# Kernel tuning notes

Measured on AMD Instinct MI355X. Metric: run time of the kernel, lower is better.

The kernel has to match this reference:

```python
import jax, jax.numpy as jnp
import numpy as np

_ALIAS = {11: 11, 13: 11, 16: 11, 21: 21, 22: 21, 23: 21, 31: 31, 32: 31, 33: 31,
          41: 41, 42: 41, 43: 41, 44: 41, 51: 51, 52: 51, 53: 51}
_COMPAT = {11: (11, 13, 16), 21: (14, 15, 21, 22, 23), 31: (15, 31, 32, 33),
           41: (41, 42, 43, 44), 51: (15, 51, 52, 53)}
_VOCAB = 64


def _tables():
    alias = np.full((_VOCAB,), -1, np.int32)
    for k, v in _ALIAS.items():
        alias[k] = v
    compat = np.zeros((_VOCAB, _VOCAB), np.float32)
    has = np.zeros((_VOCAB,), np.bool_)
    for r, toks in _COMPAT.items():
        has[r] = True
        for t in toks:
            compat[r, t] = 1.0
    return jnp.asarray(alias), jnp.asarray(compat), jnp.asarray(has)


def setup_inputs() -> dict:
    key = jax.random.key(0)
    k1, k2, k3, k4 = jax.random.split(key, 4)
    B, T, D, A, S, TTL = 8, 4096, 1024, 32, 16, 64
    H = max(TTL * 4, S * 4)
    hidden = jax.random.normal(k1, (B, T, D), jnp.float32)
    anchor_repr = jax.random.normal(k2, (B, A, D), jnp.float32)
    input_ids = jax.random.randint(k3, (B, T), 0, _VOCAB, jnp.int32)
    # end_idx in [S-1, T-H) so span start >= 0 and full horizon fits in T
    anchor_end = jax.random.randint(k4, (B, A), S - 1, T - H, jnp.int32)
    return {"hidden": hidden, "anchor_repr": anchor_repr, "input_ids": input_ids,
            "anchor_end": anchor_end, "span_len": S, "ttl": TTL}


def reference(hidden, anchor_repr, input_ids, anchor_end, span_len, ttl):
    alias_t, compat_t, has_t = _tables()
    B, T, D = hidden.shape
    A = anchor_end.shape[1]
    S = int(span_len)
    H = max(int(ttl) * 4, S * 4)
    W = H - S + 1
    eps = 1e-8

    bidx = jnp.arange(B)[:, None, None]
    start = anchor_end + 1                                   # [B,A]
    fut_idx = start[..., None] + jnp.arange(H)               # [B,A,H]
    future = hidden[bidx, fut_idx]                           # [B,A,H,D]
    fut_tok = input_ids[bidx, fut_idx]                       # [B,A,H]
    span_idx = (anchor_end - S + 1)[..., None] + jnp.arange(S)
    span = input_ids[bidx, span_idx]                         # [B,A,S]
    anchor_tok = input_ids[jnp.arange(B)[:, None], anchor_end]  # [B,A]

    # hidden-space stats (cosine_similarity with F.cosine_similarity eps)
    mean_future = future.mean(axis=2)                        # [B,A,D]
    nr = jnp.maximum(jnp.linalg.norm(anchor_repr, axis=-1), eps)
    nf = jnp.maximum(jnp.linalg.norm(mean_future, axis=-1), eps)
    sim = (anchor_repr * mean_future).sum(-1) / (nr * nf)    # [B,A]
    future_shift = jnp.linalg.norm(future - anchor_repr[:, :, None, :], axis=-1).mean(-1)
    hidden_c = jnp.maximum(0.0, (1.0 - sim) / 2.0)
    token_c = 1.0 - (fut_tok == anchor_tok[..., None]).astype(jnp.float32).mean(-1)

    # sliding windows over the horizon
    win_idx = jnp.arange(W)[:, None] + jnp.arange(S)[None, :]  # [W,S]
    win = fut_tok[:, :, win_idx]                               # [B,A,W,S]
    eq = (win == span[:, :, None, :]).astype(jnp.float32)     # [B,A,W,S]
    exact = eq.mean(-1)                                       # [B,A,W]
    pos_w = jnp.linspace(1.0, 0.4, S)
    pos_w = pos_w / pos_w.sum()
    positional = (eq * pos_w).sum(-1)

    # set-overlap: count distinct anchor tokens present in window
    eqmat = span[..., :, None] == span[..., None, :]          # [B,A,S,S]
    tri = jnp.tril(jnp.ones((S, S), bool), -1)
    first_occ = ~(eqmat & tri).any(-1)                        # first occurrence mask
    first_f = first_occ.astype(jnp.float32)
    denom = first_f.sum(-1)                                   # |set(anchor_span)|
    in_win = (win[..., :, None] == span[:, :, None, None, :]).any(-2)  # [B,A,W,S]
    overlap = (in_win.astype(jnp.float32) * first_f[:, :, None, :]).sum(-1) / denom[:, :, None]

    # infer_reference_root: first aliased token, else mode (smallest on ties)
    alias_span = alias_t[span]                                # [B,A,S], -1 if no alias
    has_a = alias_span >= 0
    first_i = jnp.argmax(has_a, -1)
    first_root = jnp.take_along_axis(alias_span, first_i[..., None], -1)[..., 0]
    counts = eqmat.sum(-1)
    maxc = counts.max(-1, keepdims=True)
    mode = jnp.where(counts == maxc, span, _VOCAB).min(-1)
    root = jnp.where(has_a.any(-1), first_root, mode)         # [B,A]

    r4 = root[:, :, None, None]
    root_pers = (win == r4).astype(jnp.float32).mean(-1)      # [B,A,W]
    alias_c = (alias_t[win] == r4).astype(jnp.float32).mean(-1)
    hard = compat_t[r4, win].mean(-1)
    regime = jnp.where(has_t[root][:, :, None],
                       0.55 * hard + 0.2 * overlap + 0.15 * alias_c + 0.1 * root_pers,
                       0.45 * exact + 0.3 * overlap + 0.1 * alias_c + 0.15 * root_pers)

    sims = 0.25 * exact + 0.15 * overlap + 0.35 * positional + 0.25 * regime
    best = sims.max(-1)
    mrp = root_pers.mean(-1)
    mrc = regime.mean(-1)
    dmass = (sims >= 0.6).astype(jnp.float32).mean(-1)
    dcoh = 0.6 * sims.mean(-1) + 0.25 * mrp + 0.15 * mrc
    pattern_c = 1.0 - (0.6 * best + 0.2 * mrp + 0.2 * mrc)

    contr = jnp.clip(0.2 * hidden_c + 0.2 * token_c + 0.6 * pattern_c, 0.0, 1.0)
    # [8,B,A]: contradiction, future_shift, similarity, hidden_c, token_c, pattern_c, mass, coherence
    return jnp.stack([contr, future_shift, sim, hidden_c, token_c, pattern_c, dmass, dcoh], 0)
```

## Files before the change

### kernel.cpp

```cpp
#include <hip/hip_runtime.h>
#include <math.h>

constexpr int kB = 8;
constexpr int kT = 4096;
constexpr int kD = 1024;
constexpr int kA = 32;
constexpr int kS = 16;
constexpr int kH = 256;
constexpr int kW = kH - kS + 1;
constexpr int NC = kD / 256;

constexpr int SPLIT = 8;
constexpr int RPS   = kH / SPLIT;
constexpr int NT1   = 256;
constexpr int NW1   = NT1 / 64;
constexpr int NWG1  = kB * kA * SPLIT;
constexpr int NT2   = 256;
constexpr int NW2   = NT2 / 64;

constexpr int NTF = 512;
constexpr int NWF = NTF / 64;

__device__ inline float wredsum(float v) {
#pragma unroll
    for (int m = 32; m >= 1; m >>= 1) v += __shfl_xor(v, m, 64);
    return v;
}
__device__ inline float wredmax(float v) {
#pragma unroll
    for (int m = 32; m >= 1; m >>= 1) v = fmaxf(v, __shfl_xor(v, m, 64));
    return v;
}

__device__ inline int alias_of(int t) {
    switch (t) {
        case 11: case 13: case 16: return 11;
        case 21: case 22: case 23: return 21;
        case 31: case 32: case 33: return 31;
        case 41: case 42: case 43: case 44: return 41;
        case 51: case 52: case 53: return 51;
        default: return -1;
    }
}

__global__ __launch_bounds__(NT1, 4) void phaseA_kernel(
    const float* __restrict__ hidden,
    const float* __restrict__ anchor_repr,
    const int*   __restrict__ anchor_end,
    float*       __restrict__ partial,
    float*       __restrict__ pshift)
{
    __shared__ float smean[NW1][kD];
    __shared__ float swshift[NW1];

    const int id = blockIdx.x;
    const int lb = (id & 7) * (NWG1 / 8) + (id >> 3);
    const int ba    = lb / SPLIT;
    const int slice = lb % SPLIT;
    const int b     = ba / kA;
    const int tid  = threadIdx.x;
    const int lane = tid & 63;
    const int wave = tid >> 6;

    const int e     = anchor_end[ba];
    const int start = e + 1;

    const float* arow = anchor_repr + (size_t)ba * kD;
    float4 anc[NC];
#pragma unroll
    for (int c = 0; c < NC; ++c) anc[c] = *(const float4*)(arow + 256 * c + 4 * lane);

    const float* hbase =
        hidden + ((size_t)b * kT + start + slice * RPS) * kD + 4 * lane;

    float sum[NC][4];
#pragma unroll
    for (int c = 0; c < NC; ++c)
#pragma unroll
        for (int j = 0; j < 4; ++j) sum[c][j] = 0.f;

    float shift_acc = 0.f;
    for (int hh = 0; hh < RPS; hh += 2 * NW1) {
        const float* r0 = hbase + (size_t)(hh + wave) * kD;
        const float* r1 = hbase + (size_t)(hh + wave + NW1) * kD;
        float ss0 = 0.f, ss1 = 0.f;
#pragma unroll
        for (int c = 0; c < NC; ++c) {
            float4 x0 = *(const float4*)(r0 + 256 * c);
            float4 x1 = *(const float4*)(r1 + 256 * c);
            float4 a  = anc[c];
            sum[c][0] += x0.x + x1.x;
            sum[c][1] += x0.y + x1.y;
            sum[c][2] += x0.z + x1.z;
            sum[c][3] += x0.w + x1.w;
            float d0 = x0.x - a.x, d1 = x0.y - a.y, d2 = x0.z - a.z, d3 = x0.w - a.w;
            float g0 = x1.x - a.x, g1 = x1.y - a.y, g2 = x1.z - a.z, g3 = x1.w - a.w;
            ss0 += d0*d0 + d1*d1 + d2*d2 + d3*d3;
            ss1 += g0*g0 + g1*g1 + g2*g2 + g3*g3;
        }
        ss0 = wredsum(ss0);
        ss1 = wredsum(ss1);
        shift_acc += sqrtf(ss0) + sqrtf(ss1);
    }
#pragma unroll
    for (int c = 0; c < NC; ++c)
        *(float4*)&smean[wave][256 * c + 4 * lane] =
            make_float4(sum[c][0], sum[c][1], sum[c][2], sum[c][3]);
    if (lane == 0) swshift[wave] = shift_acc;
    __syncthreads();

    float4 t = make_float4(0.f, 0.f, 0.f, 0.f);
#pragma unroll
    for (int w = 0; w < NW1; ++w) {
        const float4 p = *(const float4*)&smean[w][4 * tid];
        t.x += p.x; t.y += p.y; t.z += p.z; t.w += p.w;
    }
    *(float4*)(partial + ((size_t)lb << 10) + 4 * tid) = t;
    if (tid == 0) {
        float s = 0.f;
#pragma unroll
        for (int w = 0; w < NW1; ++w) s += swshift[w];
        pshift[lb] = s;
    }
}

__global__ __launch_bounds__(NT2, 1) void phaseB_kernel(
    const float* __restrict__ anchor_repr,
    const int*   __restrict__ input_ids,
    const int*   __restrict__ anchor_end,
    const float* __restrict__ partial,
    const float* __restrict__ pshift,
    float*       __restrict__ out)
{
    __shared__ int   sfut[kH];
    __shared__ int   sspan[kS];
    __shared__ float sposw[kS];
    __shared__ float sr1[NW2], sr2[NW2], sr3[NW2], sr4[NW2], sr5[NW2];
    __shared__ float s_sim, s_shift, s_hidc, s_tokc;
    __shared__ int   s_root, s_has;
    __shared__ unsigned long long s_spanmask, s_amask, s_hmask;
    __shared__ float s_denom;

    const int ba   = blockIdx.x;
    const int b    = ba / kA;
    const int tid  = threadIdx.x;
    const int lane = tid & 63;
    const int wave = tid >> 6;

    const int e     = anchor_end[ba];
    const int start = e + 1;
    const int* ids  = input_ids + b * kT;
    const int anchor_tok = ids[e];

    sfut[tid] = ids[start + tid];
    if (tid < kS) {
        sspan[tid] = ids[e - kS + 1 + tid];
        sposw[tid] = (1.0f - 0.04f * (float)tid) * (1.0f / 11.2f);
    }

    const float* arow = anchor_repr + (size_t)ba * kD;
    float4 acc = make_float4(0.f, 0.f, 0.f, 0.f);
#pragma unroll
    for (int s = 0; s < SPLIT; ++s) {
        const float4 p =
            *(const float4*)(partial + (((size_t)ba * SPLIT + s) << 10) + 4 * tid);
        acc.x += p.x; acc.y += p.y; acc.z += p.z; acc.w += p.w;
    }
    const float4 av = *(const float4*)(arow + 4 * tid);
    const float inv_h = 1.0f / (float)kH;
    float mx = acc.x * inv_h, my = acc.y * inv_h, mz = acc.z * inv_h, mw = acc.w * inv_h;
    float pm2  = mx*mx + my*my + mz*mz + mw*mw;
    float pdot = mx*av.x + my*av.y + mz*av.z + mw*av.w;
    float pa2  = av.x*av.x + av.y*av.y + av.z*av.z + av.w*av.w;
    float peq  = (sfut[tid] == anchor_tok) ? 1.f : 0.f;
    pm2 = wredsum(pm2); pdot = wredsum(pdot); pa2 = wredsum(pa2); peq = wredsum(peq);
    if (lane == 0) { sr1[wave] = pm2; sr2[wave] = pdot; sr3[wave] = pa2; sr4[wave] = peq; }
    __syncthreads();

    if (tid == 0) {
        float m2 = 0.f, dt = 0.f, a2 = 0.f, eqc = 0.f;
        for (int w = 0; w < NW2; ++w) { m2 += sr1[w]; dt += sr2[w]; a2 += sr3[w]; eqc += sr4[w]; }
        float shift = 0.f;
        for (int s = 0; s < SPLIT; ++s) shift += pshift[ba * SPLIT + s];
        float nf = fmaxf(sqrtf(m2), 1e-8f);
        float nr = fmaxf(sqrtf(a2), 1e-8f);
        float sim = dt / (nr * nf);
        s_sim   = sim;
        s_shift = shift * (1.0f / kH);
        s_hidc  = fmaxf(0.f, (1.f - sim) * 0.5f);
        s_tokc  = 1.f - eqc * (1.0f / kH);
    }
    if (tid == 64) {
        unsigned long long spanmask = 0;
        for (int s = 0; s < kS; ++s) spanmask |= 1ull << sspan[s];
        int root = -1;
        for (int s = 0; s < kS; ++s) { int al = alias_of(sspan[s]); if (al >= 0) { root = al; break; } }
        if (root < 0) {
            int counts[kS], maxc = 0;
            for (int s = 0; s < kS; ++s) {
                int c = 0;
                for (int s2 = 0; s2 < kS; ++s2) c += (sspan[s2] == sspan[s]) ? 1 : 0;
                counts[s] = c; if (c > maxc) maxc = c;
            }
            int mode = 64;
            for (int s = 0; s < kS; ++s) if (counts[s] == maxc && sspan[s] < mode) mode = sspan[s];
            root = mode;
        }
        unsigned long long am = 0, hm = 0; int has = 0;
        switch (root) {
            case 11: am = (1ull<<11)|(1ull<<13)|(1ull<<16);            hm = am;                       has = 1; break;
            case 21: am = (1ull<<21)|(1ull<<22)|(1ull<<23);            hm = am|(1ull<<14)|(1ull<<15); has = 1; break;
            case 31: am = (1ull<<31)|(1ull<<32)|(1ull<<33);            hm = am|(1ull<<15);            has = 1; break;
            case 41: am = (1ull<<41)|(1ull<<42)|(1ull<<43)|(1ull<<44); hm = am;                       has = 1; break;
            case 51: am = (1ull<<51)|(1ull<<52)|(1ull<<53);            hm = am|(1ull<<15);            has = 1; break;
            default: break;
        }
        s_root = root; s_has = has; s_spanmask = spanmask; s_amask = am; s_hmask = hm;
        s_denom = (float)__popcll(spanmask);
    }
    __syncthreads();

    const int root = s_root, has = s_has;
    const unsigned long long spanmask = s_spanmask, amask = s_amask, hmask = s_hmask;
    const float inv_denom = 1.0f / s_denom;

    float sims = -1e30f, rootpers = 0.f, regime = 0.f, simsum = 0.f, cnt = 0.f;
    if (tid < kW) {
        float wex = 0.f, wpos = 0.f, wrp = 0.f, wal = 0.f, whard = 0.f;
        unsigned long long wm = 0;
#pragma unroll
        for (int s = 0; s < kS; ++s) {
            int tok = sfut[tid + s];
            wm |= 1ull << tok;
            bool eq = (tok == sspan[s]);
            wex  += eq ? 1.f : 0.f;
            wpos += eq ? sposw[s] : 0.f;
            wrp  += (tok == root) ? 1.f : 0.f;
            wal  += ((amask >> tok) & 1ull) ? 1.f : 0.f;
            whard += ((hmask >> tok) & 1ull) ? 1.f : 0.f;
        }
        float exact  = wex * (1.f / kS);
        float overlap = (float)__popcll(wm & spanmask) * inv_denom;
        rootpers = wrp * (1.f / kS);
        float aliasc = wal * (1.f / kS);
        float hard   = whard * (1.f / kS);
        regime = has ? (0.55f*hard  + 0.2f*overlap + 0.15f*aliasc + 0.1f*rootpers)
                     : (0.45f*exact + 0.3f*overlap + 0.1f*aliasc  + 0.15f*rootpers);
        sims = 0.25f*exact + 0.15f*overlap + 0.35f*wpos + 0.25f*regime;
        simsum = sims;
        cnt = (sims >= 0.6f) ? 1.f : 0.f;
    }
    float rmax = wredmax(sims);
    float rsum = wredsum(simsum);
    float rrp  = wredsum(rootpers);
    float rreg = wredsum(regime);
    float rcnt = wredsum(cnt);
    if (lane == 0) { sr1[wave] = rmax; sr2[wave] = rsum; sr3[wave] = rrp; sr4[wave] = rreg; sr5[wave] = rcnt; }
    __syncthreads();

    if (tid == 0) {
        float best = -1e30f, ssum = 0.f, srp = 0.f, sreg = 0.f, scnt = 0.f;
        for (int w = 0; w < NW2; ++w) {
            best = fmaxf(best, sr1[w]); ssum += sr2[w]; srp += sr3[w]; sreg += sr4[w]; scnt += sr5[w];
        }
        const float invW = 1.0f / (float)kW;
        float msims = ssum * invW, mrp = srp * invW, mrc = sreg * invW, dmass = scnt * invW;
        float dcoh      = 0.6f*msims + 0.25f*mrp + 0.15f*mrc;
        float pattern_c = 1.f - (0.6f*best + 0.2f*mrp + 0.2f*mrc);
        float contr     = 0.2f*s_hidc + 0.2f*s_tokc + 0.6f*pattern_c;
        contr = fminf(fmaxf(contr, 0.f), 1.f);
        const int n = kB * kA;
        out[0*n + ba] = contr;
        out[1*n + ba] = s_shift;
        out[2*n + ba] = s_sim;
        out[3*n + ba] = s_hidc;
        out[4*n + ba] = s_tokc;
        out[5*n + ba] = pattern_c;
        out[6*n + ba] = dmass;
        out[7*n + ba] = dcoh;
    }
}

__global__ __launch_bounds__(NTF, 1) void monitor_kernel(
    const float* __restrict__ hidden,
    const float* __restrict__ anchor_repr,
    const int*   __restrict__ input_ids,
    const int*   __restrict__ anchor_end,
    float*       __restrict__ out)
{
    __shared__ float smean[NWF][kD];
    __shared__ int   sfut[kH];
    __shared__ int   sspan[kS];
    __shared__ float sposw[kS];
    __shared__ float sr1[NWF], sr2[NWF], sr3[NWF], sr4[NWF], sr5[NWF];
    __shared__ float s_sim, s_shift, s_hidc, s_tokc;
    __shared__ int   s_root, s_has;
    __shared__ unsigned long long s_spanmask, s_amask, s_hmask;
    __shared__ float s_denom;

    const int ba   = blockIdx.x;
    const int b    = ba / kA;
    const int tid  = threadIdx.x;
    const int lane = tid & 63;
    const int wave = tid >> 6;

    const int e     = anchor_end[ba];
    const int start = e + 1;
    const int* ids  = input_ids + b * kT;
    const int anchor_tok = ids[e];

    if (tid < kH) sfut[tid] = ids[start + tid];
    if (tid < kS) {
        sspan[tid] = ids[e - kS + 1 + tid];
        sposw[tid] = (1.0f - 0.04f * (float)tid) * (1.0f / 11.2f);
    }

    const float* arow = anchor_repr + (size_t)ba * kD;
    float4 anc[NC];
#pragma unroll
    for (int c = 0; c < NC; ++c) anc[c] = *(const float4*)(arow + 256 * c + 4 * lane);
    const float* hbase = hidden + ((size_t)b * kT + start) * kD + 4 * lane;

    float sum[NC][4];
#pragma unroll
    for (int c = 0; c < NC; ++c)
#pragma unroll
        for (int j = 0; j < 4; ++j) sum[c][j] = 0.f;

    float shift_acc = 0.f;
    for (int h = wave; h < kH; h += 2 * NWF) {
        const float* r0 = hbase + (size_t)h * kD;
        const float* r1 = hbase + (size_t)(h + NWF) * kD;
        float ss0 = 0.f, ss1 = 0.f;
#pragma unroll
        for (int c = 0; c < NC; ++c) {
            float4 x0 = *(const float4*)(r0 + 256 * c);
            float4 x1 = *(const float4*)(r1 + 256 * c);
            float4 a  = anc[c];
            sum[c][0] += x0.x + x1.x;
            sum[c][1] += x0.y + x1.y;
            sum[c][2] += x0.z + x1.z;
            sum[c][3] += x0.w + x1.w;
            float d0 = x0.x - a.x, d1 = x0.y - a.y, d2 = x0.z - a.z, d3 = x0.w - a.w;
            float g0 = x1.x - a.x, g1 = x1.y - a.y, g2 = x1.z - a.z, g3 = x1.w - a.w;
            ss0 += d0*d0 + d1*d1 + d2*d2 + d3*d3;
            ss1 += g0*g0 + g1*g1 + g2*g2 + g3*g3;
        }
        ss0 = wredsum(ss0);
        ss1 = wredsum(ss1);
        shift_acc += sqrtf(ss0) + sqrtf(ss1);
    }
#pragma unroll
    for (int c = 0; c < NC; ++c)
#pragma unroll
        for (int j = 0; j < 4; ++j) smean[wave][256 * c + 4 * lane + j] = sum[c][j];
    if (lane == 0) sr1[wave] = shift_acc;
    __syncthreads();

    float pm2 = 0.f, pdot = 0.f, pa2 = 0.f;
#pragma unroll
    for (int j = 0; j < kD / NTF; ++j) {
        int d = tid * (kD / NTF) + j;
        float tot = 0.f;
#pragma unroll
        for (int w2 = 0; w2 < NWF; ++w2) tot += smean[w2][d];
        float m  = tot * (1.0f / kH);
        float av = arow[d];
        pm2 += m * m; pdot += m * av; pa2 += av * av;
    }
    float peq = (tid < kH && sfut[tid] == anchor_tok) ? 1.f : 0.f;
    pm2 = wredsum(pm2); pdot = wredsum(pdot); pa2 = wredsum(pa2); peq = wredsum(peq);
    if (lane == 0) { sr2[wave] = pm2; sr3[wave] = pdot; sr4[wave] = pa2; sr5[wave] = peq; }
    __syncthreads();

    if (tid == 0) {
        float shift = 0.f, m2 = 0.f, dt = 0.f, a2 = 0.f, eqc = 0.f;
        for (int w2 = 0; w2 < NWF; ++w2) {
            shift += sr1[w2]; m2 += sr2[w2]; dt += sr3[w2]; a2 += sr4[w2]; eqc += sr5[w2];
        }
        float nf = fmaxf(sqrtf(m2), 1e-8f);
        float nr = fmaxf(sqrtf(a2), 1e-8f);
        float sim = dt / (nr * nf);
        s_sim   = sim;
        s_shift = shift * (1.0f / kH);
        s_hidc  = fmaxf(0.f, (1.f - sim) * 0.5f);
        s_tokc  = 1.f - eqc * (1.0f / kH);
    }
    if (tid == 64) {
        unsigned long long spanmask = 0;
        for (int s = 0; s < kS; ++s) spanmask |= 1ull << sspan[s];
        int root = -1;
        for (int s = 0; s < kS; ++s) { int al = alias_of(sspan[s]); if (al >= 0) { root = al; break; } }
        if (root < 0) {
            int counts[kS], maxc = 0;
            for (int s = 0; s < kS; ++s) {
                int c = 0;
                for (int s2 = 0; s2 < kS; ++s2) c += (sspan[s2] == sspan[s]) ? 1 : 0;
                counts[s] = c; if (c > maxc) maxc = c;
            }
            int mode = 64;
            for (int s = 0; s < kS; ++s) if (counts[s] == maxc && sspan[s] < mode) mode = sspan[s];
            root = mode;
        }
        unsigned long long am = 0, hm = 0; int has = 0;
        switch (root) {
            case 11: am = (1ull<<11)|(1ull<<13)|(1ull<<16);            hm = am;                       has = 1; break;
            case 21: am = (1ull<<21)|(1ull<<22)|(1ull<<23);            hm = am|(1ull<<14)|(1ull<<15); has = 1; break;
            case 31: am = (1ull<<31)|(1ull<<32)|(1ull<<33);            hm = am|(1ull<<15);            has = 1; break;
            case 41: am = (1ull<<41)|(1ull<<42)|(1ull<<43)|(1ull<<44); hm = am;                       has = 1; break;
            case 51: am = (1ull<<51)|(1ull<<52)|(1ull<<53);            hm = am|(1ull<<15);            has = 1; break;
            default: break;
        }
        s_root = root; s_has = has; s_spanmask = spanmask; s_amask = am; s_hmask = hm;
        s_denom = (float)__popcll(spanmask);
    }
    __syncthreads();

    const int root = s_root, has = s_has;
    const unsigned long long spanmask = s_spanmask, amask = s_amask, hmask = s_hmask;
    const float inv_denom = 1.0f / s_denom;

    float sims = -1e30f, rootpers = 0.f, regime = 0.f, simsum = 0.f, cnt = 0.f;
    if (tid < kW) {
        float wex = 0.f, wpos = 0.f, wrp = 0.f, wal = 0.f, whard = 0.f;
        unsigned long long wm = 0;
#pragma unroll
        for (int s = 0; s < kS; ++s) {
            int tok = sfut[tid + s];
            wm |= 1ull << tok;
            bool eq = (tok == sspan[s]);
            wex  += eq ? 1.f : 0.f;
            wpos += eq ? sposw[s] : 0.f;
            wrp  += (tok == root) ? 1.f : 0.f;
            wal  += ((amask >> tok) & 1ull) ? 1.f : 0.f;
            whard += ((hmask >> tok) & 1ull) ? 1.f : 0.f;
        }
        float exact  = wex * (1.f / kS);
        float overlap = (float)__popcll(wm & spanmask) * inv_denom;
        rootpers = wrp * (1.f / kS);
        float aliasc = wal * (1.f / kS);
        float hard   = whard * (1.f / kS);
        regime = has ? (0.55f*hard  + 0.2f*overlap + 0.15f*aliasc + 0.1f*rootpers)
                     : (0.45f*exact + 0.3f*overlap + 0.1f*aliasc  + 0.15f*rootpers);
        sims = 0.25f*exact + 0.15f*overlap + 0.35f*wpos + 0.25f*regime;
        simsum = sims;
        cnt = (sims >= 0.6f) ? 1.f : 0.f;
    }
    float rmax = wredmax(sims);
    float rsum = wredsum(simsum);
    float rrp  = wredsum(rootpers);
    float rreg = wredsum(regime);
    float rcnt = wredsum(cnt);
    if (lane == 0) { sr1[wave] = rmax; sr2[wave] = rsum; sr3[wave] = rrp; sr4[wave] = rreg; sr5[wave] = rcnt; }
    __syncthreads();

    if (tid == 0) {
        float best = -1e30f, ssum = 0.f, srp = 0.f, sreg = 0.f, scnt = 0.f;
        for (int w2 = 0; w2 < NWF; ++w2) {
            best = fmaxf(best, sr1[w2]); ssum += sr2[w2]; srp += sr3[w2]; sreg += sr4[w2]; scnt += sr5[w2];
        }
        const float invW = 1.0f / (float)kW;
        float msims = ssum * invW, mrp = srp * invW, mrc = sreg * invW, dmass = scnt * invW;
        float dcoh      = 0.6f*msims + 0.25f*mrp + 0.15f*mrc;
        float pattern_c = 1.f - (0.6f*best + 0.2f*mrp + 0.2f*mrc);
        float contr     = 0.2f*s_hidc + 0.2f*s_tokc + 0.6f*pattern_c;
        contr = fminf(fmaxf(contr, 0.f), 1.f);
        const int n = kB * kA;
        out[0*n + ba] = contr;
        out[1*n + ba] = s_shift;
        out[2*n + ba] = s_sim;
        out[3*n + ba] = s_hidc;
        out[4*n + ba] = s_tokc;
        out[5*n + ba] = pattern_c;
        out[6*n + ba] = dmass;
        out[7*n + ba] = dcoh;
    }
}

extern "C" void kernel_launch(void* const* d_in, const int* in_sizes, int n_in,
                              void* d_out, int out_size, void* d_ws, size_t ws_size,
                              hipStream_t stream) {
    const float* hidden      = (const float*)d_in[0];
    const float* anchor_repr = (const float*)d_in[1];
    const int*   input_ids   = (const int*)d_in[2];
    const int*   anchor_end  = (const int*)d_in[3];
    float* out = (float*)d_out;

    const size_t n_partial = (size_t)NWG1 * kD;
    const size_t need      = (n_partial + NWG1) * sizeof(float);

    if (d_ws != nullptr && ws_size >= need) {
        float* partial = (float*)d_ws;
        float* pshift  = partial + n_partial;
        hipLaunchKernelGGL(phaseA_kernel, dim3(NWG1), dim3(NT1), 0, stream,
                           hidden, anchor_repr, anchor_end, partial, pshift);
        hipLaunchKernelGGL(phaseB_kernel, dim3(kB * kA), dim3(NT2), 0, stream,
                           anchor_repr, input_ids, anchor_end, partial, pshift, out);
    } else {
        hipLaunchKernelGGL(monitor_kernel, dim3(kB * kA), dim3(NTF), 0, stream,
                           hidden, anchor_repr, input_ids, anchor_end, out);
    }
}
```

Baseline: 215.1 us.

## Tile hidden rows per batch and share loads across overlapping anchor windows

The first stage is restructured so that each block owns a fixed 128-row tile of one batch's hidden states, not one slice of one anchor's window. The block loads each row once and accumulates it into every anchor window that covers it, up to eight anchors per pass, keeping the anchor vectors in shared memory. The aim is to remove the redundant global reads caused by overlapping 256-row windows. The cost is more branching, several block-wide syncs per anchor pair, and serial passes when many anchors hit one tile. The second stage and the fallback kernel move to 1024-thread blocks and sum up to three partials per anchor.

```diff
diff --git a/kernel.cpp b/kernel.cpp
--- a/kernel.cpp
+++ b/kernel.cpp
@@ -8,18 +8,14 @@
 constexpr int kS = 16;
 constexpr int kH = 256;
 constexpr int kW = kH - kS + 1;
+constexpr int kBA = kB * kA;
+constexpr int kRB = 128;
+constexpr int kNJ = kT / kRB;
+constexpr int kMK = 3;
 constexpr int NC = kD / 256;
 
-constexpr int SPLIT = 8;
-constexpr int RPS   = kH / SPLIT;
-constexpr int NT1   = 256;
-constexpr int NW1   = NT1 / 64;
-constexpr int NWG1  = kB * kA * SPLIT;
-constexpr int NT2   = 256;
-constexpr int NW2   = NT2 / 64;
-
-constexpr int NTF = 512;
-constexpr int NWF = NTF / 64;
+constexpr int NT = 1024;
+constexpr int NW = NT / 64;
 
 __device__ inline float wredsum(float v) {
 #pragma unroll
@@ -43,88 +39,136 @@
     }
 }
 
-__global__ __launch_bounds__(NT1, 4) void phaseA_kernel(
+__global__ __launch_bounds__(NT) void s1_kernel(
     const float* __restrict__ hidden,
     const float* __restrict__ anchor_repr,
     const int*   __restrict__ anchor_end,
     float*       __restrict__ partial,
     float*       __restrict__ pshift)
 {
-    __shared__ float smean[NW1][kD];
-    __shared__ float swshift[NW1];
+    __shared__ float lanc[8][kD];
+    __shared__ float comb[NW][kD];
+    __shared__ float ssh[NW];
 
     const int id = blockIdx.x;
-    const int lb = (id & 7) * (NWG1 / 8) + (id >> 3);
-    const int ba    = lb / SPLIT;
-    const int slice = lb % SPLIT;
-    const int b     = ba / kA;
+    const int b  = id & 7;
+    const int j  = id >> 3;
     const int tid  = threadIdx.x;
     const int lane = tid & 63;
     const int wave = tid >> 6;
-
-    const int e     = anchor_end[ba];
-    const int start = e + 1;
-
-    const float* arow = anchor_repr + (size_t)ba * kD;
-    float4 anc[NC];
-#pragma unroll
-    for (int c = 0; c < NC; ++c) anc[c] = *(const float4*)(arow + 256 * c + 4 * lane);
-
-    const float* hbase =
-        hidden + ((size_t)b * kT + start + slice * RPS) * kD + 4 * lane;
-
-    float sum[NC][4];
-#pragma unroll
-    for (int c = 0; c < NC; ++c)
-#pragma unroll
-        for (int j = 0; j < 4; ++j) sum[c][j] = 0.f;
-
-    float shift_acc = 0.f;
-    for (int hh = 0; hh < RPS; hh += 2 * NW1) {
-        const float* r0 = hbase + (size_t)(hh + wave) * kD;
-        const float* r1 = hbase + (size_t)(hh + wave + NW1) * kD;
-        float ss0 = 0.f, ss1 = 0.f;
-#pragma unroll
-        for (int c = 0; c < NC; ++c) {
-            float4 x0 = *(const float4*)(r0 + 256 * c);
-            float4 x1 = *(const float4*)(r1 + 256 * c);
-            float4 a  = anc[c];
-            sum[c][0] += x0.x + x1.x;
-            sum[c][1] += x0.y + x1.y;
-            sum[c][2] += x0.z + x1.z;
-            sum[c][3] += x0.w + x1.w;
-            float d0 = x0.x - a.x, d1 = x0.y - a.y, d2 = x0.z - a.z, d3 = x0.w - a.w;
-            float g0 = x1.x - a.x, g1 = x1.y - a.y, g2 = x1.z - a.z, g3 = x1.w - a.w;
-            ss0 += d0*d0 + d1*d1 + d2*d2 + d3*d3;
-            ss1 += g0*g0 + g1*g1 + g2*g2 + g3*g3;
-        }
-        ss0 = wredsum(ss0);
-        ss1 = wredsum(ss1);
-        shift_acc += sqrtf(ss0) + sqrtf(ss1);
-    }
-#pragma unroll
-    for (int c = 0; c < NC; ++c)
-        *(float4*)&smean[wave][256 * c + 4 * lane] =
-            make_float4(sum[c][0], sum[c][1], sum[c][2], sum[c][3]);
-    if (lane == 0) swshift[wave] = shift_acc;
-    __syncthreads();
-
-    float4 t = make_float4(0.f, 0.f, 0.f, 0.f);
-#pragma unroll
-    for (int w = 0; w < NW1; ++w) {
-        const float4 p = *(const float4*)&smean[w][4 * tid];
-        t.x += p.x; t.y += p.y; t.z += p.z; t.w += p.w;
-    }
-    *(float4*)(partial + ((size_t)lb << 10) + 4 * tid) = t;
-    if (tid == 0) {
-        float s = 0.f;
-#pragma unroll
-        for (int w = 0; w < NW1; ++w) s += swshift[w];
-        pshift[lb] = s;
-    }
-}
-
-__global__ __launch_bounds__(NT2, 1) void phaseB_kernel(
+    const int g  = wave >> 3;
+    const int ww = wave & 7;
+    const int r0 = j * kRB;
+
+    const int* ae = anchor_end + b * kA;
+    unsigned mask = 0;
+    for (int a = 0; a < kA; ++a) {
+        int st = ae[a] + 1;
+        if ((st >> 7) <= j && j <= ((st + kH - 1) >> 7)) mask |= 1u << a;
+    }
+
+    const float* hbase = hidden + ((size_t)(b * kT + r0)) * kD + 4 * lane;
+
+    while (mask) {
+        int aidx[8], stv[8];
+        int npass = 0;
+        unsigned rem = mask;
+#pragma unroll
+        for (int s = 0; s < 8; ++s) {
+            if (rem) { aidx[s] = __ffs((int)rem) - 1; rem &= rem - 1u; ++npass; }
+            else       aidx[s] = -1;
+            stv[s] = (aidx[s] >= 0) ? (ae[aidx[s]] + 1) : 0x40000000;
+        }
+        mask = rem;
+
+#pragma unroll
+        for (int s = 0; s < 8; ++s)
+            if (aidx[s] >= 0)
+                lanc[s][tid] = anchor_repr[((size_t)(b * kA + aidx[s])) * kD + tid];
+        __syncthreads();
+
+        int stc[4];
+#pragma unroll
+        for (int c = 0; c < 4; ++c) stc[c] = g ? stv[2 * c + 1] : stv[2 * c];
+
+        float4 vs[4][NC];
+#pragma unroll
+        for (int c = 0; c < 4; ++c)
+#pragma unroll
+            for (int ch = 0; ch < NC; ++ch) vs[c][ch] = make_float4(0.f, 0.f, 0.f, 0.f);
+        float sacc[4] = {0.f, 0.f, 0.f, 0.f};
+
+        for (int t = 0; t < kRB / 8; ++t) {
+            const int lr = ww + 8 * t;
+            const int r  = r0 + lr;
+            const bool in0 = ((unsigned)(r - stc[0]) < (unsigned)kH);
+            const bool in1 = ((unsigned)(r - stc[1]) < (unsigned)kH);
+            const bool in2 = ((unsigned)(r - stc[2]) < (unsigned)kH);
+            const bool in3 = ((unsigned)(r - stc[3]) < (unsigned)kH);
+            if (!(in0 | in1 | in2 | in3)) continue;
+            float4 x[NC];
+#pragma unroll
+            for (int ch = 0; ch < NC; ++ch)
+                x[ch] = *(const float4*)(hbase + (size_t)lr * kD + 256 * ch);
+            const bool inc[4] = {in0, in1, in2, in3};
+#pragma unroll
+            for (int c = 0; c < 4; ++c) {
+                if (inc[c]) {
+                    const float* ap = &lanc[2 * c + g][4 * lane];
+                    float acc = 0.f;
+#pragma unroll
+                    for (int ch = 0; ch < NC; ++ch) {
+                        float4 a4 = *(const float4*)(ap + 256 * ch);
+                        vs[c][ch].x += x[ch].x; vs[c][ch].y += x[ch].y;
+                        vs[c][ch].z += x[ch].z; vs[c][ch].w += x[ch].w;
+                        float d0 = x[ch].x - a4.x, d1 = x[ch].y - a4.y;
+                        float d2 = x[ch].z - a4.z, d3 = x[ch].w - a4.w;
+                        acc += d0*d0 + d1*d1 + d2*d2 + d3*d3;
+                    }
+#pragma unroll
+                    for (int m = 32; m >= 1; m >>= 1) acc += __shfl_xor(acc, m, 64);
+                    sacc[c] += sqrtf(acc);
+                }
+            }
+        }
+
+#pragma unroll
+        for (int c = 0; c < 4; ++c) {
+            __syncthreads();
+#pragma unroll
+            for (int ch = 0; ch < NC; ++ch)
+                *(float4*)&comb[wave][256 * ch + 4 * lane] = vs[c][ch];
+            if (lane == 0) ssh[wave] = sacc[c];
+            __syncthreads();
+            float s0 = 0.f, s1 = 0.f;
+#pragma unroll
+            for (int w = 0; w < 8; ++w) { s0 += comb[w][tid]; s1 += comb[8 + w][tid]; }
+            if (2 * c < npass) {
+                const int ba0 = b * kA + aidx[2 * c];
+                const int k0  = j - (stv[2 * c] >> 7);
+                partial[((size_t)(ba0 * kMK + k0) << 10) + tid] = s0;
+            }
+            if (2 * c + 1 < npass) {
+                const int ba1 = b * kA + aidx[2 * c + 1];
+                const int k1  = j - (stv[2 * c + 1] >> 7);
+                partial[((size_t)(ba1 * kMK + k1) << 10) + tid] = s1;
+            }
+            if (tid == 0 && 2 * c < npass) {
+                float t0 = 0.f;
+                for (int w = 0; w < 8; ++w) t0 += ssh[w];
+                pshift[(b * kA + aidx[2 * c]) * kMK + (j - (stv[2 * c] >> 7))] = t0;
+            }
+            if (tid == 64 && 2 * c + 1 < npass) {
+                float t1 = 0.f;
+                for (int w = 8; w < 16; ++w) t1 += ssh[w];
+                pshift[(b * kA + aidx[2 * c + 1]) * kMK + (j - (stv[2 * c + 1] >> 7))] = t1;
+            }
+        }
+        __syncthreads();
+    }
+}
+
+__global__ __launch_bounds__(NT) void s2_kernel(
     const float* __restrict__ anchor_repr,
     const int*   __restrict__ input_ids,
     const int*   __restrict__ anchor_end,
@@ -135,7 +179,7 @@
     __shared__ int   sfut[kH];
     __shared__ int   sspan[kS];
     __shared__ float sposw[kS];
-    __shared__ float sr1[NW2], sr2[NW2], sr3[NW2], sr4[NW2], sr5[NW2];
+    __shared__ float sr1[NW], sr2[NW], sr3[NW], sr4[NW], sr5[NW];
     __shared__ float s_sim, s_shift, s_hidc, s_tokc;
     __shared__ int   s_root, s_has;
     __shared__ unsigned long long s_spanmask, s_amask, s_hmask;
@@ -152,36 +196,32 @@
     const int* ids  = input_ids + b * kT;
     const int anchor_tok = ids[e];
 
-    sfut[tid] = ids[start + tid];
+    if (tid < kH) sfut[tid] = ids[start + tid];
     if (tid < kS) {
         sspan[tid] = ids[e - kS + 1 + tid];
         sposw[tid] = (1.0f - 0.04f * (float)tid) * (1.0f / 11.2f);
     }
 
     const float* arow = anchor_repr + (size_t)ba * kD;
-    float4 acc = make_float4(0.f, 0.f, 0.f, 0.f);
-#pragma unroll
-    for (int s = 0; s < SPLIT; ++s) {
-        const float4 p =
-            *(const float4*)(partial + (((size_t)ba * SPLIT + s) << 10) + 4 * tid);
-        acc.x += p.x; acc.y += p.y; acc.z += p.z; acc.w += p.w;
-    }
-    const float4 av = *(const float4*)(arow + 4 * tid);
-    const float inv_h = 1.0f / (float)kH;
-    float mx = acc.x * inv_h, my = acc.y * inv_h, mz = acc.z * inv_h, mw = acc.w * inv_h;
-    float pm2  = mx*mx + my*my + mz*mz + mw*mw;
-    float pdot = mx*av.x + my*av.y + mz*av.z + mw*av.w;
-    float pa2  = av.x*av.x + av.y*av.y + av.z*av.z + av.w*av.w;
-    float peq  = (sfut[tid] == anchor_tok) ? 1.f : 0.f;
+    const int nk = ((start + kH - 1) >> 7) - (start >> 7) + 1;
+    float tot = 0.f;
+    for (int k = 0; k < nk; ++k)
+        tot += partial[((size_t)(ba * kMK + k) << 10) + tid];
+    float m  = tot * (1.0f / kH);
+    float av = arow[tid];
+    float pm2  = m * m;
+    float pdot = m * av;
+    float pa2  = av * av;
+    float peq  = (tid < kH && sfut[tid] == anchor_tok) ? 1.f : 0.f;
     pm2 = wredsum(pm2); pdot = wredsum(pdot); pa2 = wredsum(pa2); peq = wredsum(peq);
-    if (lane == 0) { sr1[wave] = pm2; sr2[wave] = pdot; sr3[wave] = pa2; sr4[wave] = peq; }
+    if (lane == 0) { sr2[wave] = pm2; sr3[wave] = pdot; sr4[wave] = pa2; sr5[wave] = peq; }
     __syncthreads();
 
     if (tid == 0) {
         float m2 = 0.f, dt = 0.f, a2 = 0.f, eqc = 0.f;
-        for (int w = 0; w < NW2; ++w) { m2 += sr1[w]; dt += sr2[w]; a2 += sr3[w]; eqc += sr4[w]; }
+        for (int w = 0; w < NW; ++w) { m2 += sr2[w]; dt += sr3[w]; a2 += sr4[w]; eqc += sr5[w]; }
         float shift = 0.f;
-        for (int s = 0; s < SPLIT; ++s) shift += pshift[ba * SPLIT + s];
+        for (int k = 0; k < nk; ++k) shift += pshift[ba * kMK + k];
         float nf = fmaxf(sqrtf(m2), 1e-8f);
         float nr = fmaxf(sqrtf(a2), 1e-8f);
         float sim = dt / (nr * nf);
@@ -260,7 +300,7 @@
 
     if (tid == 0) {
         float best = -1e30f, ssum = 0.f, srp = 0.f, sreg = 0.f, scnt = 0.f;
-        for (int w = 0; w < NW2; ++w) {
+        for (int w = 0; w < NW; ++w) {
             best = fmaxf(best, sr1[w]); ssum += sr2[w]; srp += sr3[w]; sreg += sr4[w]; scnt += sr5[w];
         }
         const float invW = 1.0f / (float)kW;
@@ -281,25 +321,26 @@
     }
 }
 
-__global__ __launch_bounds__(NTF, 1) void monitor_kernel(
+__global__ __launch_bounds__(NT) void monitor_kernel(
     const float* __restrict__ hidden,
     const float* __restrict__ anchor_repr,
     const int*   __restrict__ input_ids,
     const int*   __restrict__ anchor_end,
     float*       __restrict__ out)
 {
-    __shared__ float smean[NWF][kD];
+    __shared__ float smean[NW][kD];
     __shared__ int   sfut[kH];
     __shared__ int   sspan[kS];
     __shared__ float sposw[kS];
-    __shared__ float sr1[NWF], sr2[NWF], sr3[NWF], sr4[NWF], sr5[NWF];
+    __shared__ float sr1[NW], sr2[NW], sr3[NW], sr4[NW], sr5[NW];
     __shared__ float s_sim, s_shift, s_hidc, s_tokc;
     __shared__ int   s_root, s_has;
     __shared__ unsigned long long s_spanmask, s_amask, s_hmask;
     __shared__ float s_denom;
 
-    const int ba   = blockIdx.x;
-    const int b    = ba / kA;
+    const int id = blockIdx.x;
+    const int ba = (id & 7) * 32 + (id >> 3);
+    const int b  = ba / kA;
     const int tid  = threadIdx.x;
     const int lane = tid & 63;
     const int wave = tid >> 6;
@@ -327,56 +368,56 @@
 #pragma unroll
         for (int j = 0; j < 4; ++j) sum[c][j] = 0.f;
 
+    float ss[kH / NW];
+#pragma unroll
+    for (int k = 0; k < kH / NW; ++k) ss[k] = 0.f;
+#pragma unroll
+    for (int k = 0; k < kH / NW; ++k) {
+        const float* rp = hbase + (size_t)(wave + NW * k) * kD;
+        float acc = 0.f;
+#pragma unroll
+        for (int c = 0; c < NC; ++c) {
+            float4 x = *(const float4*)(rp + 256 * c);
+            float4 a = anc[c];
+            sum[c][0] += x.x; sum[c][1] += x.y; sum[c][2] += x.z; sum[c][3] += x.w;
+            float d0 = x.x - a.x, d1 = x.y - a.y, d2 = x.z - a.z, d3 = x.w - a.w;
+            acc += d0*d0 + d1*d1 + d2*d2 + d3*d3;
+        }
+        ss[k] = acc;
+    }
+#pragma unroll
+    for (int m = 32; m >= 1; m >>= 1) {
+#pragma unroll
+        for (int k = 0; k < kH / NW; ++k) ss[k] += __shfl_xor(ss[k], m, 64);
+    }
     float shift_acc = 0.f;
-    for (int h = wave; h < kH; h += 2 * NWF) {
-        const float* r0 = hbase + (size_t)h * kD;
-        const float* r1 = hbase + (size_t)(h + NWF) * kD;
-        float ss0 = 0.f, ss1 = 0.f;
-#pragma unroll
-        for (int c = 0; c < NC; ++c) {
-            float4 x0 = *(const float4*)(r0 + 256 * c);
-            float4 x1 = *(const float4*)(r1 + 256 * c);
-            float4 a  = anc[c];
-            sum[c][0] += x0.x + x1.x;
-            sum[c][1] += x0.y + x1.y;
-            sum[c][2] += x0.z + x1.z;
-            sum[c][3] += x0.w + x1.w;
-            float d0 = x0.x - a.x, d1 = x0.y - a.y, d2 = x0.z - a.z, d3 = x0.w - a.w;
-            float g0 = x1.x - a.x, g1 = x1.y - a.y, g2 = x1.z - a.z, g3 = x1.w - a.w;
-            ss0 += d0*d0 + d1*d1 + d2*d2 + d3*d3;
-            ss1 += g0*g0 + g1*g1 + g2*g2 + g3*g3;
-        }
-        ss0 = wredsum(ss0);
-        ss1 = wredsum(ss1);
-        shift_acc += sqrtf(ss0) + sqrtf(ss1);
-    }
+#pragma unroll
+    for (int k = 0; k < kH / NW; ++k) shift_acc += sqrtf(ss[k]);
+
 #pragma unroll
     for (int c = 0; c < NC; ++c)
-#pragma unroll
-        for (int j = 0; j < 4; ++j) smean[wave][256 * c + 4 * lane + j] = sum[c][j];
+        *(float4*)&smean[wave][256 * c + 4 * lane] =
+            make_float4(sum[c][0], sum[c][1], sum[c][2], sum[c][3]);
     if (lane == 0) sr1[wave] = shift_acc;
     __syncthreads();
 
-    float pm2 = 0.f, pdot = 0.f, pa2 = 0.f;
-#pragma unroll
-    for (int j = 0; j < kD / NTF; ++j) {
-        int d = tid * (kD / NTF) + j;
-        float tot = 0.f;
-#pragma unroll
-        for (int w2 = 0; w2 < NWF; ++w2) tot += smean[w2][d];
-        float m  = tot * (1.0f / kH);
-        float av = arow[d];
-        pm2 += m * m; pdot += m * av; pa2 += av * av;
-    }
-    float peq = (tid < kH && sfut[tid] == anchor_tok) ? 1.f : 0.f;
+    float tot = 0.f;
+#pragma unroll
+    for (int w = 0; w < NW; ++w) tot += smean[w][tid];
+    float m  = tot * (1.0f / kH);
+    float av = arow[tid];
+    float pm2  = m * m;
+    float pdot = m * av;
+    float pa2  = av * av;
+    float peq  = (tid < kH && sfut[tid] == anchor_tok) ? 1.f : 0.f;
     pm2 = wredsum(pm2); pdot = wredsum(pdot); pa2 = wredsum(pa2); peq = wredsum(peq);
     if (lane == 0) { sr2[wave] = pm2; sr3[wave] = pdot; sr4[wave] = pa2; sr5[wave] = peq; }
     __syncthreads();
 
     if (tid == 0) {
         float shift = 0.f, m2 = 0.f, dt = 0.f, a2 = 0.f, eqc = 0.f;
-        for (int w2 = 0; w2 < NWF; ++w2) {
-            shift += sr1[w2]; m2 += sr2[w2]; dt += sr3[w2]; a2 += sr4[w2]; eqc += sr5[w2];
+        for (int w = 0; w < NW; ++w) {
+            shift += sr1[w]; m2 += sr2[w]; dt += sr3[w]; a2 += sr4[w]; eqc += sr5[w];
         }
         float nf = fmaxf(sqrtf(m2), 1e-8f);
         float nr = fmaxf(sqrtf(a2), 1e-8f);
@@ -456,8 +497,8 @@
 
     if (tid == 0) {
         float best = -1e30f, ssum = 0.f, srp = 0.f, sreg = 0.f, scnt = 0.f;
-        for (int w2 = 0; w2 < NWF; ++w2) {
-            best = fmaxf(best, sr1[w2]); ssum += sr2[w2]; srp += sr3[w2]; sreg += sr4[w2]; scnt += sr5[w2];
+        for (int w = 0; w < NW; ++w) {
+            best = fmaxf(best, sr1[w]); ssum += sr2[w]; srp += sr3[w]; sreg += sr4[w]; scnt += sr5[w];
         }
         const float invW = 1.0f / (float)kW;
         float msims = ssum * invW, mrp = srp * invW, mrc = sreg * invW, dmass = scnt * invW;
@@ -486,18 +527,18 @@
     const int*   anchor_end  = (const int*)d_in[3];
     float* out = (float*)d_out;
 
-    const size_t n_partial = (size_t)NWG1 * kD;
-    const size_t need      = (n_partial + NWG1) * sizeof(float);
+    const size_t n_partial = (size_t)kBA * kMK * kD;
+    const size_t need      = (n_partial + kBA * kMK) * sizeof(float);
 
     if (d_ws != nullptr && ws_size >= need) {
         float* partial = (float*)d_ws;
         float* pshift  = partial + n_partial;
-        hipLaunchKernelGGL(phaseA_kernel, dim3(NWG1), dim3(NT1), 0, stream,
+        hipLaunchKernelGGL(s1_kernel, dim3(kB * kNJ), dim3(NT), 0, stream,
                            hidden, anchor_repr, anchor_end, partial, pshift);
-        hipLaunchKernelGGL(phaseB_kernel, dim3(kB * kA), dim3(NT2), 0, stream,
+        hipLaunchKernelGGL(s2_kernel, dim3(kBA), dim3(NT), 0, stream,
                            anchor_repr, input_ids, anchor_end, partial, pshift, out);
     } else {
-        hipLaunchKernelGGL(monitor_kernel, dim3(kB * kA), dim3(NTF), 0, stream,
+        hipLaunchKernelGGL(monitor_kernel, dim3(kBA), dim3(NT), 0, stream,
                            hidden, anchor_repr, input_ids, anchor_end, out);
     }
 }
```

After: 230.2 us. 7.0% more time.
